# Kernel optimization log

Hardware: AMD Instinct MI355X
Metric: run time of the kernel (lower is better)

The kernel has to match this reference:

```python
import jax, jax.numpy as jnp
import numpy as np

BETA = 0.5
ITEM_NUM = 100000
REGION_NUM = 1000
EMBED = 128
HIDDEN = 256
B, H = 1024, 256


def setup_inputs() -> dict:
    key = jax.random.key(0)
    ks = jax.random.split(key, 10)
    history = jax.random.randint(ks[0], (B, H), 0, ITEM_NUM)
    target = jax.random.randint(ks[1], (B,), 0, ITEM_NUM)
    history_region = jax.random.randint(ks[2], (B, H), 0, REGION_NUM)
    target_region = jax.random.randint(ks[3], (B,), 0, REGION_NUM)
    E_hist = 0.01 * jax.random.normal(ks[4], (ITEM_NUM, EMBED), dtype=jnp.float32)
    E_targ = 0.01 * jax.random.normal(ks[5], (ITEM_NUM, EMBED), dtype=jnp.float32)
    E_reg = 0.01 * jax.random.normal(ks[6], (REGION_NUM, EMBED), dtype=jnp.float32)
    lim1 = 1.0 / np.sqrt(2 * EMBED)
    W1 = jax.random.uniform(ks[7], (2 * EMBED, HIDDEN), jnp.float32, -lim1, lim1)
    b1 = jnp.zeros((HIDDEN,), jnp.float32)
    lim2 = 1.0 / np.sqrt(HIDDEN)
    w2 = jax.random.uniform(ks[8], (HIDDEN,), jnp.float32, -lim2, lim2)
    return {"history": history, "target": target,
            "history_region": history_region, "target_region": target_region,
            "E_hist": E_hist, "E_targ": E_targ, "E_reg": E_reg,
            "W1": W1, "b1": b1, "w2": w2}


def reference(history, target, history_region, target_region,
              E_hist, E_targ, E_reg, W1, b1, w2):
    # gathers + concat: hist [B,H,2d], tgt [B,2d]
    hist = jnp.concatenate([E_hist[history], E_reg[history_region]], axis=-1)
    tgt = jnp.concatenate([E_targ[target], E_reg[target_region]], axis=-1)
    # elementwise product broadcast over history dim
    inp = hist * tgt[:, None, :]                      # [B,H,2d]
    hid = jax.nn.relu(jnp.einsum('bhd,dk->bhk', inp, W1) + b1)
    scores = jnp.einsum('bhk,k->bh', hid, w2)         # [B,H]
    mask = (history != target[:, None]).astype(scores.dtype)
    exp_a = jnp.exp(scores) * mask                    # [B,H]
    denom = jnp.power(jnp.sum(exp_a, axis=-1), BETA)  # [B]
    attn = exp_a / denom[:, None]                     # [B,H]
    # weighted reduction: sum_h sum_d hist*attn*tgt
    pred = jnp.einsum('bhd,bh,bd->b', hist, attn, tgt)
    return jax.nn.sigmoid(pred)
```

## Files before the change

kernel.cpp:

```cpp
#include <hip/hip_runtime.h>
#include <hip/hip_bf16.h>

#define NB 1024
#define NH 256
#define EMB 128
#define TWOD 256
#define HID 256
#define ROWS 128
#define BPB 2
#define NBLK (NB * BPB)

typedef __attribute__((ext_vector_type(4))) float f32x4;
typedef __attribute__((ext_vector_type(8))) short bf16x8;

__device__ __forceinline__ unsigned short f2bf(float f) {
  union { float f; unsigned u; } v; v.f = f;
  unsigned u = v.u;
  unsigned r = (u + 0x7fffu + ((u >> 16) & 1u)) >> 16;
  return (unsigned short)r;
}

__global__ __launch_bounds__(256) void prep_w1t(const float* __restrict__ W1,
                                                unsigned short* __restrict__ W1T) {
  const int d = blockIdx.x;
  const int n = threadIdx.x;
  W1T[(size_t)n * TWOD + d] = f2bf(W1[(size_t)d * HID + n]);
}

__global__ __launch_bounds__(512, 4) void nais_main(
    const int* __restrict__ history, const int* __restrict__ target,
    const int* __restrict__ hregion, const int* __restrict__ tregion,
    const float* __restrict__ E_hist, const float* __restrict__ E_targ,
    const float* __restrict__ E_reg,
    const unsigned short* __restrict__ W1T, const float* __restrict__ b1,
    const float* __restrict__ w2,
    float* __restrict__ part_se, float* __restrict__ part_sd)
{
  const int blk = blockIdx.x;
  const int b = blk >> 1;
  const int r0 = (blk & 1) * ROWS;
  const int tid = threadIdx.x;
  const int lane = tid & 63;
  const int wave = tid >> 6;
  const int l15 = lane & 15;
  const int lhi = lane >> 4;
  const int l31 = lane & 31;
  const int halfsel = lane >> 5;

  __shared__ __align__(16) unsigned short inp_lds[ROWS * 256];
  __shared__ float dot_lds[ROWS];
  __shared__ int items_lds[ROWS];
  __shared__ float score_parts[8][ROWS];

  const float* tsrc = halfsel ? (E_reg + (size_t)tregion[b] * EMB)
                              : (E_targ + (size_t)target[b] * EMB);
  const f32x4 t = *(const f32x4*)(tsrc + l31 * 4);
  const int tgt_item = target[b];

  const int* keysrc = halfsel ? hregion : history;
  const float* table = halfsel ? E_reg : E_hist;

  {
    int key[16];
    #pragma unroll
    for (int s = 0; s < 16; ++s)
      key[s] = keysrc[b * NH + r0 + wave * 16 + s];

    #pragma unroll
    for (int pass = 0; pass < 2; ++pass) {
      f32x4 vb[8];
      #pragma unroll
      for (int s = 0; s < 8; ++s)
        vb[s] = *(const f32x4*)(table + (size_t)key[pass * 8 + s] * EMB + l31 * 4);

      #pragma unroll
      for (int s = 0; s < 8; ++s) {
        const int row = wave * 16 + pass * 8 + s;
        if (lane == 0) items_lds[row] = key[pass * 8 + s];
        f32x4 v = vb[s] * t;
        float ds = v[0] + v[1] + v[2] + v[3];
        ds += __shfl_xor(ds, 1);
        ds += __shfl_xor(ds, 2);
        ds += __shfl_xor(ds, 4);
        ds += __shfl_xor(ds, 8);
        ds += __shfl_xor(ds, 16);
        ds += __shfl_xor(ds, 32);
        if (lane == 0) dot_lds[row] = ds;

        float2 f01; f01.x = v[0]; f01.y = v[1];
        float2 f23; f23.x = v[2]; f23.y = v[3];
        __hip_bfloat162 p0 = __float22bfloat162_rn(f01);
        __hip_bfloat162 p1 = __float22bfloat162_rn(f23);
        union { __hip_bfloat162 h; unsigned u; } c0, c1;
        c0.h = p0; c1.h = p1;
        const int g = halfsel * 16 + (l31 >> 1);
        const int gs = g ^ (row & 7) ^ ((g >> 3) & 3);
        unsigned* dst = (unsigned*)&inp_lds[row * 256 + gs * 8 + (lane & 1) * 4];
        dst[0] = c0.u; dst[1] = c1.u;
      }
    }
  }
  __syncthreads();

  {
    const int col0 = wave * 32;
    float b1v[2], w2v[2];
    #pragma unroll
    for (int n = 0; n < 2; ++n) {
      const int colh = col0 + n * 16 + l15;
      b1v[n] = b1[colh];
      w2v[n] = w2[colh];
    }

    f32x4 acc[2][4][2];
    #pragma unroll
    for (int c = 0; c < 2; ++c)
      #pragma unroll
      for (int m = 0; m < 4; ++m)
        #pragma unroll
        for (int n = 0; n < 2; ++n)
          acc[c][m][n] = (f32x4){0.f, 0.f, 0.f, 0.f};

    #pragma unroll
    for (int kk = 0; kk < 8; ++kk) {
      bf16x8 bfr[2];
      #pragma unroll
      for (int n = 0; n < 2; ++n) {
        const int colh = col0 + n * 16 + l15;
        bfr[n] = *(const bf16x8*)(W1T + (size_t)colh * TWOD + kk * 32 + lhi * 8);
      }
      bf16x8 af[2][4];
      #pragma unroll
      for (int c = 0; c < 2; ++c)
        #pragma unroll
        for (int m = 0; m < 4; ++m) {
          const int row = c * 64 + m * 16 + l15;
          const int gk = kk * 4 + lhi;
          const int gs = gk ^ (row & 7) ^ ((gk >> 3) & 3);
          af[c][m] = *(const bf16x8*)(&inp_lds[row * 256 + gs * 8]);
        }
      __builtin_amdgcn_s_setprio(1);
      #pragma unroll
      for (int c = 0; c < 2; ++c)
        #pragma unroll
        for (int m = 0; m < 4; ++m)
          #pragma unroll
          for (int n = 0; n < 2; ++n)
            acc[c][m][n] = __builtin_amdgcn_mfma_f32_16x16x32_bf16(af[c][m], bfr[n], acc[c][m][n], 0, 0, 0);
      __builtin_amdgcn_s_setprio(0);
    }

    #pragma unroll
    for (int c = 0; c < 2; ++c) {
      #pragma unroll
      for (int m = 0; m < 4; ++m) {
        #pragma unroll
        for (int r = 0; r < 4; ++r) {
          float p = 0.f;
          #pragma unroll
          for (int n = 0; n < 2; ++n) {
            float hv = acc[c][m][n][r] + b1v[n];
            hv = hv > 0.f ? hv : 0.f;
            p += hv * w2v[n];
          }
          p += __shfl_xor(p, 1);
          p += __shfl_xor(p, 2);
          p += __shfl_xor(p, 4);
          p += __shfl_xor(p, 8);
          if (l15 == 0) score_parts[wave][c * 64 + m * 16 + lhi * 4 + r] = p;
        }
      }
    }
  }
  __syncthreads();

  if (wave < 2) {
    const int lrow = wave * 64 + lane;
    float sc = 0.f;
    #pragma unroll
    for (int w = 0; w < 8; ++w) sc += score_parts[w][lrow];
    float e = (items_lds[lrow] != tgt_item) ? expf(sc) : 0.f;
    float ed = e * dot_lds[lrow];
    #pragma unroll
    for (int off = 32; off >= 1; off >>= 1) {
      e += __shfl_xor(e, off);
      ed += __shfl_xor(ed, off);
    }
    if (lane == 0) {
      part_se[blk * 2 + wave] = e;
      part_sd[blk * 2 + wave] = ed;
    }
  }
}

__global__ __launch_bounds__(256) void finalize(const float* __restrict__ part_se,
                                                const float* __restrict__ part_sd,
                                                float* __restrict__ out) {
  const int b = blockIdx.x * 256 + threadIdx.x;
  if (b < NB) {
    float se = 0.f, sd = 0.f;
    #pragma unroll
    for (int i = 0; i < BPB * 2; ++i) {
      se += part_se[b * BPB * 2 + i];
      sd += part_sd[b * BPB * 2 + i];
    }
    const float pred = (se > 0.f) ? (sd / sqrtf(se)) : 0.f;
    out[b] = 1.f / (1.f + expf(-pred));
  }
}

extern "C" void kernel_launch(void* const* d_in, const int* in_sizes, int n_in,
                              void* d_out, int out_size, void* d_ws, size_t ws_size,
                              hipStream_t stream) {
  const int* history = (const int*)d_in[0];
  const int* target  = (const int*)d_in[1];
  const int* hregion = (const int*)d_in[2];
  const int* tregion = (const int*)d_in[3];
  const float* E_hist = (const float*)d_in[4];
  const float* E_targ = (const float*)d_in[5];
  const float* E_reg  = (const float*)d_in[6];
  const float* W1 = (const float*)d_in[7];
  const float* b1 = (const float*)d_in[8];
  const float* w2 = (const float*)d_in[9];
  float* out = (float*)d_out;

  char* p = (char*)d_ws;
  unsigned short* W1T = (unsigned short*)p;  p += (size_t)TWOD * HID * 2;
  float* part_se = (float*)p;                p += (size_t)NBLK * 2 * 4;
  float* part_sd = (float*)p;

  prep_w1t<<<TWOD, HID, 0, stream>>>(W1, W1T);
  nais_main<<<NBLK, 512, 0, stream>>>(history, target, hregion, tregion,
                                      E_hist, E_targ, E_reg, W1T, b1, w2,
                                      part_se, part_sd);
  finalize<<<(NB + 255) / 256, 256, 0, stream>>>(part_se, part_sd, out);
}
```

Before: 87.54 us.

## Fuse finalize into main kernel via last-block counter, tile W1 transpose

Removes the separate finalize launch by having each block bump a global atomic counter; the last block to finish sums the partials and writes the sigmoid outputs. The W1 transpose kernel now goes through a shared-memory tile so both its reads and writes are coalesced, and it launches 16 blocks instead of 256. History and region keys are staged once in LDS rather than loaded per wave. The trade is an added memset, threadfences and an extra barrier in every block, plus a serial tail where one block does the whole final reduction.

```diff
diff --git a/kernel.cpp b/kernel.cpp
--- a/kernel.cpp
+++ b/kernel.cpp
@@ -22,9 +22,22 @@
 
 __global__ __launch_bounds__(256) void prep_w1t(const float* __restrict__ W1,
                                                 unsigned short* __restrict__ W1T) {
-  const int d = blockIdx.x;
-  const int n = threadIdx.x;
-  W1T[(size_t)n * TWOD + d] = f2bf(W1[(size_t)d * HID + n]);
+  const int bx = blockIdx.x & 3;
+  const int by = blockIdx.x >> 2;
+  __shared__ float tile[64][65];
+  const int tr = threadIdx.x >> 6;
+  const int tc = threadIdx.x & 63;
+  #pragma unroll
+  for (int i = 0; i < 16; ++i) {
+    const int d = bx * 64 + i * 4 + tr;
+    tile[i * 4 + tr][tc] = W1[(size_t)d * HID + by * 64 + tc];
+  }
+  __syncthreads();
+  #pragma unroll
+  for (int i = 0; i < 16; ++i) {
+    const int n = by * 64 + i * 4 + tr;
+    W1T[(size_t)n * TWOD + bx * 64 + tc] = f2bf(tile[tc][i * 4 + tr]);
+  }
 }
 
 __global__ __launch_bounds__(512, 4) void nais_main(
@@ -34,7 +47,8 @@
     const float* __restrict__ E_reg,
     const unsigned short* __restrict__ W1T, const float* __restrict__ b1,
     const float* __restrict__ w2,
-    float* __restrict__ part_se, float* __restrict__ part_sd)
+    float* __restrict__ part_se, float* __restrict__ part_sd,
+    unsigned* __restrict__ counter, float* __restrict__ out)
 {
   const int blk = blockIdx.x;
   const int b = blk >> 1;
@@ -49,55 +63,61 @@
 
   __shared__ __align__(16) unsigned short inp_lds[ROWS * 256];
   __shared__ float dot_lds[ROWS];
-  __shared__ int items_lds[ROWS];
+  __shared__ int keys_h[ROWS];
+  __shared__ int keys_r[ROWS];
   __shared__ float score_parts[8][ROWS];
+  __shared__ unsigned is_last;
 
   const float* tsrc = halfsel ? (E_reg + (size_t)tregion[b] * EMB)
                               : (E_targ + (size_t)target[b] * EMB);
   const f32x4 t = *(const f32x4*)(tsrc + l31 * 4);
   const int tgt_item = target[b];
 
-  const int* keysrc = halfsel ? hregion : history;
+  if (tid < ROWS) {
+    keys_h[tid] = history[b * NH + r0 + tid];
+  } else if (tid < 2 * ROWS) {
+    keys_r[tid - ROWS] = hregion[b * NH + r0 + (tid - ROWS)];
+  }
+  __syncthreads();
+
   const float* table = halfsel ? E_reg : E_hist;
-
-  {
-    int key[16];
-    #pragma unroll
-    for (int s = 0; s < 16; ++s)
-      key[s] = keysrc[b * NH + r0 + wave * 16 + s];
-
-    #pragma unroll
-    for (int pass = 0; pass < 2; ++pass) {
-      f32x4 vb[8];
-      #pragma unroll
-      for (int s = 0; s < 8; ++s)
-        vb[s] = *(const f32x4*)(table + (size_t)key[pass * 8 + s] * EMB + l31 * 4);
-
-      #pragma unroll
-      for (int s = 0; s < 8; ++s) {
-        const int row = wave * 16 + pass * 8 + s;
-        if (lane == 0) items_lds[row] = key[pass * 8 + s];
-        f32x4 v = vb[s] * t;
-        float ds = v[0] + v[1] + v[2] + v[3];
-        ds += __shfl_xor(ds, 1);
-        ds += __shfl_xor(ds, 2);
-        ds += __shfl_xor(ds, 4);
-        ds += __shfl_xor(ds, 8);
-        ds += __shfl_xor(ds, 16);
-        ds += __shfl_xor(ds, 32);
-        if (lane == 0) dot_lds[row] = ds;
-
-        float2 f01; f01.x = v[0]; f01.y = v[1];
-        float2 f23; f23.x = v[2]; f23.y = v[3];
-        __hip_bfloat162 p0 = __float22bfloat162_rn(f01);
-        __hip_bfloat162 p1 = __float22bfloat162_rn(f23);
-        union { __hip_bfloat162 h; unsigned u; } c0, c1;
-        c0.h = p0; c1.h = p1;
-        const int g = halfsel * 16 + (l31 >> 1);
-        const int gs = g ^ (row & 7) ^ ((g >> 3) & 3);
-        unsigned* dst = (unsigned*)&inp_lds[row * 256 + gs * 8 + (lane & 1) * 4];
-        dst[0] = c0.u; dst[1] = c1.u;
-      }
+  const int* keys = halfsel ? keys_r : keys_h;
+
+  #pragma unroll
+  for (int pass = 0; pass < 2; ++pass) {
+    int key8[8];
+    #pragma unroll
+    for (int s = 0; s < 8; ++s)
+      key8[s] = keys[wave * 16 + pass * 8 + s];
+
+    f32x4 vb[8];
+    #pragma unroll
+    for (int s = 0; s < 8; ++s)
+      vb[s] = *(const f32x4*)(table + (size_t)key8[s] * EMB + l31 * 4);
+
+    #pragma unroll
+    for (int s = 0; s < 8; ++s) {
+      const int row = wave * 16 + pass * 8 + s;
+      f32x4 v = vb[s] * t;
+      float ds = v[0] + v[1] + v[2] + v[3];
+      ds += __shfl_xor(ds, 1);
+      ds += __shfl_xor(ds, 2);
+      ds += __shfl_xor(ds, 4);
+      ds += __shfl_xor(ds, 8);
+      ds += __shfl_xor(ds, 16);
+      ds += __shfl_xor(ds, 32);
+      if (lane == 0) dot_lds[row] = ds;
+
+      float2 f01; f01.x = v[0]; f01.y = v[1];
+      float2 f23; f23.x = v[2]; f23.y = v[3];
+      __hip_bfloat162 p0 = __float22bfloat162_rn(f01);
+      __hip_bfloat162 p1 = __float22bfloat162_rn(f23);
+      union { __hip_bfloat162 h; unsigned u; } c0, c1;
+      c0.h = p0; c1.h = p1;
+      const int g = halfsel * 16 + (l31 >> 1);
+      const int gs = g ^ (row & 7) ^ ((g >> 3) & 3);
+      unsigned* dst = (unsigned*)&inp_lds[row * 256 + gs * 8 + (lane & 1) * 4];
+      dst[0] = c0.u; dst[1] = c1.u;
     }
   }
   __syncthreads();
@@ -179,7 +199,7 @@
     float sc = 0.f;
     #pragma unroll
     for (int w = 0; w < 8; ++w) sc += score_parts[w][lrow];
-    float e = (items_lds[lrow] != tgt_item) ? expf(sc) : 0.f;
+    float e = (keys_h[lrow] != tgt_item) ? expf(sc) : 0.f;
     float ed = e * dot_lds[lrow];
     #pragma unroll
     for (int off = 32; off >= 1; off >>= 1) {
@@ -191,21 +211,28 @@
       part_sd[blk * 2 + wave] = ed;
     }
   }
-}
-
-__global__ __launch_bounds__(256) void finalize(const float* __restrict__ part_se,
-                                                const float* __restrict__ part_sd,
-                                                float* __restrict__ out) {
-  const int b = blockIdx.x * 256 + threadIdx.x;
-  if (b < NB) {
-    float se = 0.f, sd = 0.f;
-    #pragma unroll
-    for (int i = 0; i < BPB * 2; ++i) {
-      se += part_se[b * BPB * 2 + i];
-      sd += part_sd[b * BPB * 2 + i];
-    }
-    const float pred = (se > 0.f) ? (sd / sqrtf(se)) : 0.f;
-    out[b] = 1.f / (1.f + expf(-pred));
+
+  __threadfence();
+  __syncthreads();
+  if (tid == 0) {
+    const unsigned old = atomicAdd(counter, 1u);
+    is_last = (old == (unsigned)(NBLK - 1)) ? 1u : 0u;
+  }
+  __syncthreads();
+  if (is_last) {
+    __threadfence();
+    #pragma unroll
+    for (int i = 0; i < 2; ++i) {
+      const int bb = i * 512 + tid;
+      float se = 0.f, sd = 0.f;
+      #pragma unroll
+      for (int j = 0; j < BPB * 2; ++j) {
+        se += part_se[bb * BPB * 2 + j];
+        sd += part_sd[bb * BPB * 2 + j];
+      }
+      const float pred = (se > 0.f) ? (sd / sqrtf(se)) : 0.f;
+      out[bb] = 1.f / (1.f + expf(-pred));
+    }
   }
 }
 
@@ -227,11 +254,12 @@
   char* p = (char*)d_ws;
   unsigned short* W1T = (unsigned short*)p;  p += (size_t)TWOD * HID * 2;
   float* part_se = (float*)p;                p += (size_t)NBLK * 2 * 4;
-  float* part_sd = (float*)p;
-
-  prep_w1t<<<TWOD, HID, 0, stream>>>(W1, W1T);
+  float* part_sd = (float*)p;                p += (size_t)NBLK * 2 * 4;
+  unsigned* counter = (unsigned*)p;
+
+  hipMemsetAsync(counter, 0, sizeof(unsigned), stream);
+  prep_w1t<<<16, 256, 0, stream>>>(W1, W1T);
   nais_main<<<NBLK, 512, 0, stream>>>(history, target, hregion, tregion,
                                       E_hist, E_targ, E_reg, W1T, b1, w2,
-                                      part_se, part_sd);
-  finalize<<<(NB + 255) / 256, 256, 0, stream>>>(part_se, part_sd, out);
-}
+                                      part_se, part_sd, counter, out);
+}
```

New measurement: 315.2 us. 260% more time.
